# Kernel tuning notes

Measured on AMD Instinct MI355X. Metric: run time of the kernel, lower is better.

## Reference

```python
import jax, jax.numpy as jnp
import numpy as np

B_, NX, NY = 32, 512, 512


def _grad(f, axis):
    # torch.gradient(dim=axis, edge_order=2), unit spacing
    f = jnp.moveaxis(f, axis, -1)
    g = (jnp.roll(f, -1, axis=-1) - jnp.roll(f, 1, axis=-1)) * 0.5
    g0 = -1.5 * f[..., 0] + 2.0 * f[..., 1] - 0.5 * f[..., 2]
    gN = 1.5 * f[..., -1] - 2.0 * f[..., -2] + 0.5 * f[..., -3]
    g = g.at[..., 0].set(g0).at[..., -1].set(gN)
    return jnp.moveaxis(g, -1, axis)


def _grad2(f, axis):
    # roll-based 2nd derivative with one-sided 2nd-order boundary stencils
    f = jnp.moveaxis(f, axis, -1)
    g = jnp.roll(f, -1, axis=-1) - 2.0 * f + jnp.roll(f, 1, axis=-1)
    g0 = 2.0 * f[..., 0] - 5.0 * f[..., 1] + 4.0 * f[..., 2] - f[..., 3]
    gN = 2.0 * f[..., -1] - 5.0 * f[..., -2] + 4.0 * f[..., -3] - f[..., -4]
    g = g.at[..., 0].set(g0).at[..., -1].set(gN)
    return jnp.moveaxis(g, -1, axis)


def setup_inputs() -> dict:
    key = jax.random.key(0)
    k1, k2, k3, k4 = jax.random.split(key, 4)
    f = jax.random.uniform(k1, (B_, NX, NY), dtype=jnp.float32)
    dt = jax.random.uniform(k2, (B_,), dtype=jnp.float32)
    A = jax.random.normal(k3, (B_, 2, NX, NY), dtype=jnp.float32)
    B = jax.random.normal(k4, (B_, 3, NX, NY), dtype=jnp.float32)
    return {"f": f, "dt": dt, "A": A, "B": B}


def reference(f, dt, A, B):
    # Fokker-Planck explicit update: f' = f + dt * (-div(Af) + 0.5 * div^2(Bf))
    Af = A * f[:, None]            # [B, 2, Nx, Ny]
    Bf = B * f[:, None]            # [B, 3, Nx, Ny]
    gradv_Af = _grad(Af[:, 0], 1) + _grad(Af[:, 1], 2)
    gradvv_Bf = (_grad2(Bf[:, 0], 1) + _grad2(Bf[:, 1], 2)
                 + _grad(_grad(Bf[:, 2], 2), 1)
                 + _grad(_grad(Bf[:, 2], 1), 2))
    df = -gradv_Af + gradvv_Bf * 0.5
    f_new = f + df * dt[:, None, None]
    return jnp.maximum(f_new, 0.0)  # ensure_non_negative_f
```

## Files before the change

### kernel.cpp

```cpp
#include <hip/hip_runtime.h>


constexpr int NXc = 512;
constexpr int NYc = 512;
constexpr int NBc = 32;

struct Win { float m1, v0, v1, v2, v3, p4; };

__device__ __forceinline__ float4 mul4(float4 p, float4 q) {
    float4 r; r.x = p.x*q.x; r.y = p.y*q.y; r.z = p.z*q.z; r.w = p.w*q.w; return r;
}
__device__ __forceinline__ float4 fma4s(float s, float4 p, float4 acc) {
    acc.x = fmaf(s, p.x, acc.x); acc.y = fmaf(s, p.y, acc.y);
    acc.z = fmaf(s, p.z, acc.z); acc.w = fmaf(s, p.w, acc.w); return acc;
}
__device__ __forceinline__ float4 add4(float4 a, float4 b) {
    float4 r; r.x = a.x+b.x; r.y = a.y+b.y; r.z = a.z+b.z; r.w = a.w+b.w; return r;
}

__device__ __forceinline__ Win mkwin(float4 a, float am1, float ap4,
                                     float4 fv, float fm1, float fp4) {
    Win w;
    w.m1 = am1 * fm1;
    w.v0 = a.x * fv.x; w.v1 = a.y * fv.y; w.v2 = a.z * fv.z; w.v3 = a.w * fv.w;
    w.p4 = ap4 * fp4;
    return w;
}

__device__ __forceinline__ float4 dy4(const Win& w, bool atY0, bool atYN) {
    float4 r;
    r.x = atY0 ? (-1.5f*w.v0 + 2.0f*w.v1 - 0.5f*w.v2) : 0.5f*(w.v1 - w.m1);
    r.y = 0.5f*(w.v2 - w.v0);
    r.z = 0.5f*(w.v3 - w.v1);
    r.w = atYN ? (1.5f*w.v3 - 2.0f*w.v2 + 0.5f*w.v1) : 0.5f*(w.p4 - w.v2);
    return r;
}
__device__ __forceinline__ float4 dyy4(const Win& w, bool atY0, bool atYN) {
    float4 r;
    r.x = atY0 ? (2.0f*w.v0 - 5.0f*w.v1 + 4.0f*w.v2 - w.v3) : (w.v1 - 2.0f*w.v0 + w.m1);
    r.y = w.v2 - 2.0f*w.v1 + w.v0;
    r.z = w.v3 - 2.0f*w.v2 + w.v1;
    r.w = atYN ? (2.0f*w.v3 - 5.0f*w.v2 + 4.0f*w.v1 - w.v0) : (w.p4 - 2.0f*w.v3 + w.v2);
    return r;
}

__global__ __launch_bounds__(128) void fp2d_kernel(
    const float* __restrict__ f,
    const float* __restrict__ dt,
    const float* __restrict__ A,
    const float* __restrict__ Bm,
    float* __restrict__ out)
{
    const int x  = blockIdx.x & (NXc - 1);
    const int b  = blockIdx.x >> 9;
    const int y4 = threadIdx.x << 2;

    const bool atY0 = (y4 == 0);
    const bool atYN = (y4 == NYc - 4);
    const int ym1 = atY0 ? 0 : y4 - 1;
    const int yp4 = atYN ? NYc - 1 : y4 + 4;

    const size_t plane = (size_t)NXc * NYc;
    const float* fb = f  + (size_t)b * plane;
    const float* A0 = A  + (size_t)b * 2 * plane;
    const float* A1 = A0 + plane;
    const float* B0 = Bm + (size_t)b * 3 * plane;
    const float* B1 = B0 + plane;
    const float* B2 = B1 + plane;

    int xa, xb_, xc, u3; float wxa, wxb, wxc, v0, v1, v2, v3;
    if (x == 0) {
        xa = 0; xb_ = 1; xc = 2; u3 = 3;
        wxa = -1.5f; wxb = 2.0f; wxc = -0.5f;
        v0 = 2.0f; v1 = -5.0f; v2 = 4.0f; v3 = -1.0f;
    } else if (x == NXc - 1) {
        xa = NXc - 1; xb_ = NXc - 2; xc = NXc - 3; u3 = NXc - 4;
        wxa = 1.5f; wxb = -2.0f; wxc = 0.5f;
        v0 = 2.0f; v1 = -5.0f; v2 = 4.0f; v3 = -1.0f;
    } else {
        xa = x - 1; xb_ = x; xc = x + 1; u3 = x;
        wxa = -0.5f; wxb = 0.0f; wxc = 0.5f;
        v0 = 1.0f; v1 = -2.0f; v2 = 1.0f; v3 = 0.0f;
    }
    const bool xInt = (x > 0) && (x < NXc - 1);

    auto ld4 = [](const float* p, int row, int col) -> float4 {
        return *reinterpret_cast<const float4*>(p + (size_t)row * NYc + col);
    };
    auto ld1 = [](const float* p, int row, int col) -> float {
        return p[(size_t)row * NYc + col];
    };

    float4 f_a = ld4(fb, xa, y4);  float fam = ld1(fb, xa, ym1), fap = ld1(fb, xa, yp4);
    float4 f_b = ld4(fb, xb_, y4); float fbm = ld1(fb, xb_, ym1), fbp = ld1(fb, xb_, yp4);
    float4 f_c = ld4(fb, xc, y4);  float fcm = ld1(fb, xc, ym1), fcp = ld1(fb, xc, yp4);
    float4 f_u = ld4(fb, u3, y4);

    float4 fX = xInt ? f_b : f_a;
    float  fXm = xInt ? fbm : fam;
    float  fXp = xInt ? fbp : fap;

    float4 a0a = ld4(A0, xa, y4), a0b = ld4(A0, xb_, y4), a0c = ld4(A0, xc, y4);
    float4 a1x = ld4(A1, x,  y4); float a1m = ld1(A1, x, ym1), a1p = ld1(A1, x, yp4);

    float4 b0a = ld4(B0, xa, y4), b0b = ld4(B0, xb_, y4), b0c = ld4(B0, xc, y4), b0u = ld4(B0, u3, y4);
    float4 b1x = ld4(B1, x,  y4); float b1m = ld1(B1, x, ym1), b1p = ld1(B1, x, yp4);

    float4 b2a = ld4(B2, xa, y4);  float b2am = ld1(B2, xa, ym1), b2ap = ld1(B2, xa, yp4);
    float4 b2b = ld4(B2, xb_, y4); float b2bm = ld1(B2, xb_, ym1), b2bp = ld1(B2, xb_, yp4);
    float4 b2c = ld4(B2, xc, y4);  float b2cm = ld1(B2, xc, ym1), b2cp = ld1(B2, xc, yp4);

    float4 zero; zero.x = zero.y = zero.z = zero.w = 0.0f;
    float4 gradv = fma4s(wxa, mul4(a0a, f_a),
                   fma4s(wxb, mul4(a0b, f_b),
                   fma4s(wxc, mul4(a0c, f_c), zero)));
    Win wA1 = mkwin(a1x, a1m, a1p, fX, fXm, fXp);
    gradv = add4(gradv, dy4(wA1, atY0, atYN));

    float4 dxx = fma4s(v0, mul4(b0a, f_a),
                 fma4s(v1, mul4(b0b, f_b),
                 fma4s(v2, mul4(b0c, f_c),
                 fma4s(v3, mul4(b0u, f_u), zero))));

    Win wB1 = mkwin(b1x, b1m, b1p, fX, fXm, fXp);
    float4 dyy = dyy4(wB1, atY0, atYN);

    Win wB2a = mkwin(b2a, b2am, b2ap, f_a, fam, fap);
    Win wB2b = mkwin(b2b, b2bm, b2bp, f_b, fbm, fbp);
    Win wB2c = mkwin(b2c, b2cm, b2cp, f_c, fcm, fcp);
    float4 cross = fma4s(wxa, dy4(wB2a, atY0, atYN),
                   fma4s(wxb, dy4(wB2b, atY0, atYN),
                   fma4s(wxc, dy4(wB2c, atY0, atYN), zero)));

    const float dtb = dt[b];
    float4 res;
    {
        float dfx = 0.5f*(dxx.x + dyy.x) + cross.x - gradv.x;
        float dfy = 0.5f*(dxx.y + dyy.y) + cross.y - gradv.y;
        float dfz = 0.5f*(dxx.z + dyy.z) + cross.z - gradv.z;
        float dfw = 0.5f*(dxx.w + dyy.w) + cross.w - gradv.w;
        res.x = fmaxf(fmaf(dfx, dtb, fX.x), 0.0f);
        res.y = fmaxf(fmaf(dfy, dtb, fX.y), 0.0f);
        res.z = fmaxf(fmaf(dfz, dtb, fX.z), 0.0f);
        res.w = fmaxf(fmaf(dfw, dtb, fX.w), 0.0f);
    }

    *reinterpret_cast<float4*>(out + (size_t)b * plane + (size_t)x * NYc + y4) = res;
}

extern "C" void kernel_launch(void* const* d_in, const int* in_sizes, int n_in,
                              void* d_out, int out_size, void* d_ws, size_t ws_size,
                              hipStream_t stream) {
    const float* f  = (const float*)d_in[0];
    const float* dt = (const float*)d_in[1];
    const float* A  = (const float*)d_in[2];
    const float* Bm = (const float*)d_in[3];
    float* out = (float*)d_out;

    const int blocks = NBc * NXc;
    fp2d_kernel<<<blocks, 128, 0, stream>>>(f, dt, A, Bm, out);
}
```

Measured before the change: 238.5 us.

## Map one wavefront per row with 8 columns per lane and shuffle halos

Each 64-lane wavefront now covers a full 512-wide row, with each lane holding 8 contiguous columns, and a block of 256 threads covers 4 rows. Halo neighbours in y are exchanged with wavefront shuffles instead of extra scalar global loads, which removes about a dozen redundant scalar loads per thread. The block count drops by four and each thread keeps more data in registers, which raises register pressure. Edge lanes hold garbage shuffle values, but those are overridden by the one-sided boundary stencils.

```diff
diff --git a/kernel.cpp b/kernel.cpp
--- a/kernel.cpp
+++ b/kernel.cpp
@@ -5,7 +5,7 @@
 constexpr int NYc = 512;
 constexpr int NBc = 32;
 
-struct Win { float m1, v0, v1, v2, v3, p4; };
+struct F8 { float4 lo, hi; };
 
 __device__ __forceinline__ float4 mul4(float4 p, float4 q) {
     float4 r; r.x = p.x*q.x; r.y = p.y*q.y; r.z = p.z*q.z; r.w = p.w*q.w; return r;
@@ -14,51 +14,81 @@
     acc.x = fmaf(s, p.x, acc.x); acc.y = fmaf(s, p.y, acc.y);
     acc.z = fmaf(s, p.z, acc.z); acc.w = fmaf(s, p.w, acc.w); return acc;
 }
-__device__ __forceinline__ float4 add4(float4 a, float4 b) {
-    float4 r; r.x = a.x+b.x; r.y = a.y+b.y; r.z = a.z+b.z; r.w = a.w+b.w; return r;
+__device__ __forceinline__ F8 mul8(const F8& a, const F8& b) {
+    F8 r; r.lo = mul4(a.lo, b.lo); r.hi = mul4(a.hi, b.hi); return r;
+}
+__device__ __forceinline__ F8 fma8s(float s, const F8& p, const F8& acc) {
+    F8 r; r.lo = fma4s(s, p.lo, acc.lo); r.hi = fma4s(s, p.hi, acc.hi); return r;
+}
+__device__ __forceinline__ F8 add8(const F8& a, const F8& b) {
+    F8 r;
+    r.lo.x = a.lo.x+b.lo.x; r.lo.y = a.lo.y+b.lo.y; r.lo.z = a.lo.z+b.lo.z; r.lo.w = a.lo.w+b.lo.w;
+    r.hi.x = a.hi.x+b.hi.x; r.hi.y = a.hi.y+b.hi.y; r.hi.z = a.hi.z+b.hi.z; r.hi.w = a.hi.w+b.hi.w;
+    return r;
 }
 
-__device__ __forceinline__ Win mkwin(float4 a, float am1, float ap4,
-                                     float4 fv, float fm1, float fp4) {
-    Win w;
-    w.m1 = am1 * fm1;
-    w.v0 = a.x * fv.x; w.v1 = a.y * fv.y; w.v2 = a.z * fv.z; w.v3 = a.w * fv.w;
-    w.p4 = ap4 * fp4;
+__device__ __forceinline__ F8 ld8(const float* __restrict__ p, int row, int y8) {
+    const float* q = p + (size_t)row * NYc + y8;
+    F8 r;
+    r.lo = *reinterpret_cast<const float4*>(q);
+    r.hi = *reinterpret_cast<const float4*>(q + 4);
+    return r;
+}
+
+struct W8 { float4 lo, hi; float m1, p8; };
+
+__device__ __forceinline__ W8 mkwin8(const F8& a, const F8& f) {
+    W8 w;
+    w.lo = mul4(a.lo, f.lo);
+    w.hi = mul4(a.hi, f.hi);
+    w.m1 = __shfl_up(w.hi.w, 1);
+    w.p8 = __shfl_down(w.lo.x, 1);
     return w;
 }
 
-__device__ __forceinline__ float4 dy4(const Win& w, bool atY0, bool atYN) {
-    float4 r;
-    r.x = atY0 ? (-1.5f*w.v0 + 2.0f*w.v1 - 0.5f*w.v2) : 0.5f*(w.v1 - w.m1);
-    r.y = 0.5f*(w.v2 - w.v0);
-    r.z = 0.5f*(w.v3 - w.v1);
-    r.w = atYN ? (1.5f*w.v3 - 2.0f*w.v2 + 0.5f*w.v1) : 0.5f*(w.p4 - w.v2);
+__device__ __forceinline__ F8 dy8(const W8& w, bool atY0, bool atYN) {
+    F8 r;
+    r.lo.x = atY0 ? (-1.5f*w.lo.x + 2.0f*w.lo.y - 0.5f*w.lo.z) : 0.5f*(w.lo.y - w.m1);
+    r.lo.y = 0.5f*(w.lo.z - w.lo.x);
+    r.lo.z = 0.5f*(w.lo.w - w.lo.y);
+    r.lo.w = 0.5f*(w.hi.x - w.lo.z);
+    r.hi.x = 0.5f*(w.hi.y - w.lo.w);
+    r.hi.y = 0.5f*(w.hi.z - w.hi.x);
+    r.hi.z = 0.5f*(w.hi.w - w.hi.y);
+    r.hi.w = atYN ? (1.5f*w.hi.w - 2.0f*w.hi.z + 0.5f*w.hi.y) : 0.5f*(w.p8 - w.hi.z);
     return r;
 }
-__device__ __forceinline__ float4 dyy4(const Win& w, bool atY0, bool atYN) {
-    float4 r;
-    r.x = atY0 ? (2.0f*w.v0 - 5.0f*w.v1 + 4.0f*w.v2 - w.v3) : (w.v1 - 2.0f*w.v0 + w.m1);
-    r.y = w.v2 - 2.0f*w.v1 + w.v0;
-    r.z = w.v3 - 2.0f*w.v2 + w.v1;
-    r.w = atYN ? (2.0f*w.v3 - 5.0f*w.v2 + 4.0f*w.v1 - w.v0) : (w.p4 - 2.0f*w.v3 + w.v2);
+__device__ __forceinline__ F8 dyy8(const W8& w, bool atY0, bool atYN) {
+    F8 r;
+    r.lo.x = atY0 ? (2.0f*w.lo.x - 5.0f*w.lo.y + 4.0f*w.lo.z - w.lo.w)
+                  : (w.lo.y - 2.0f*w.lo.x + w.m1);
+    r.lo.y = w.lo.z - 2.0f*w.lo.y + w.lo.x;
+    r.lo.z = w.lo.w - 2.0f*w.lo.z + w.lo.y;
+    r.lo.w = w.hi.x - 2.0f*w.lo.w + w.lo.z;
+    r.hi.x = w.hi.y - 2.0f*w.hi.x + w.lo.w;
+    r.hi.y = w.hi.z - 2.0f*w.hi.y + w.hi.x;
+    r.hi.z = w.hi.w - 2.0f*w.hi.z + w.hi.y;
+    r.hi.w = atYN ? (2.0f*w.hi.w - 5.0f*w.hi.z + 4.0f*w.hi.y - w.hi.x)
+                  : (w.p8 - 2.0f*w.hi.w + w.hi.z);
     return r;
 }
 
-__global__ __launch_bounds__(128) void fp2d_kernel(
+__global__ __launch_bounds__(256) void fp2d_kernel(
     const float* __restrict__ f,
     const float* __restrict__ dt,
     const float* __restrict__ A,
     const float* __restrict__ Bm,
     float* __restrict__ out)
 {
-    const int x  = blockIdx.x & (NXc - 1);
-    const int b  = blockIdx.x >> 9;
-    const int y4 = threadIdx.x << 2;
+    const int tid  = threadIdx.x;
+    const int wv   = tid >> 6;
+    const int lane = tid & 63;
+    const int b    = blockIdx.x >> 7;
+    const int x    = ((blockIdx.x & 127) << 2) + wv;
+    const int y8   = lane << 3;
 
-    const bool atY0 = (y4 == 0);
-    const bool atYN = (y4 == NYc - 4);
-    const int ym1 = atY0 ? 0 : y4 - 1;
-    const int yp4 = atYN ? NYc - 1 : y4 + 4;
+    const bool atY0 = (lane == 0);
+    const bool atYN = (lane == 63);
 
     const size_t plane = (size_t)NXc * NYc;
     const float* fb = f  + (size_t)b * plane;
@@ -84,68 +114,59 @@
     }
     const bool xInt = (x > 0) && (x < NXc - 1);
 
-    auto ld4 = [](const float* p, int row, int col) -> float4 {
-        return *reinterpret_cast<const float4*>(p + (size_t)row * NYc + col);
-    };
-    auto ld1 = [](const float* p, int row, int col) -> float {
-        return p[(size_t)row * NYc + col];
-    };
+    F8 f_a = ld8(fb, xa, y8);
+    F8 f_b = ld8(fb, xb_, y8);
+    F8 f_c = ld8(fb, xc, y8);
+    F8 f_u = ld8(fb, u3, y8);
 
-    float4 f_a = ld4(fb, xa, y4);  float fam = ld1(fb, xa, ym1), fap = ld1(fb, xa, yp4);
-    float4 f_b = ld4(fb, xb_, y4); float fbm = ld1(fb, xb_, ym1), fbp = ld1(fb, xb_, yp4);
-    float4 f_c = ld4(fb, xc, y4);  float fcm = ld1(fb, xc, ym1), fcp = ld1(fb, xc, yp4);
-    float4 f_u = ld4(fb, u3, y4);
+    F8 a0a = ld8(A0, xa, y8), a0b = ld8(A0, xb_, y8), a0c = ld8(A0, xc, y8);
+    F8 a1x = ld8(A1, x, y8);
+    F8 b0a = ld8(B0, xa, y8), b0b = ld8(B0, xb_, y8), b0c = ld8(B0, xc, y8), b0u = ld8(B0, u3, y8);
+    F8 b1x = ld8(B1, x, y8);
+    F8 b2a = ld8(B2, xa, y8), b2b = ld8(B2, xb_, y8), b2c = ld8(B2, xc, y8);
 
-    float4 fX = xInt ? f_b : f_a;
-    float  fXm = xInt ? fbm : fam;
-    float  fXp = xInt ? fbp : fap;
+    F8 fX;
+    fX.lo = xInt ? f_b.lo : f_a.lo;
+    fX.hi = xInt ? f_b.hi : f_a.hi;
 
-    float4 a0a = ld4(A0, xa, y4), a0b = ld4(A0, xb_, y4), a0c = ld4(A0, xc, y4);
-    float4 a1x = ld4(A1, x,  y4); float a1m = ld1(A1, x, ym1), a1p = ld1(A1, x, yp4);
+    F8 zero8; zero8.lo = make_float4(0.f,0.f,0.f,0.f); zero8.hi = zero8.lo;
 
-    float4 b0a = ld4(B0, xa, y4), b0b = ld4(B0, xb_, y4), b0c = ld4(B0, xc, y4), b0u = ld4(B0, u3, y4);
-    float4 b1x = ld4(B1, x,  y4); float b1m = ld1(B1, x, ym1), b1p = ld1(B1, x, yp4);
+    F8 gradv = fma8s(wxa, mul8(a0a, f_a),
+               fma8s(wxb, mul8(a0b, f_b),
+               fma8s(wxc, mul8(a0c, f_c), zero8)));
+    W8 wA1 = mkwin8(a1x, fX);
+    gradv = add8(gradv, dy8(wA1, atY0, atYN));
 
-    float4 b2a = ld4(B2, xa, y4);  float b2am = ld1(B2, xa, ym1), b2ap = ld1(B2, xa, yp4);
-    float4 b2b = ld4(B2, xb_, y4); float b2bm = ld1(B2, xb_, ym1), b2bp = ld1(B2, xb_, yp4);
-    float4 b2c = ld4(B2, xc, y4);  float b2cm = ld1(B2, xc, ym1), b2cp = ld1(B2, xc, yp4);
+    F8 dxx = fma8s(v0, mul8(b0a, f_a),
+             fma8s(v1, mul8(b0b, f_b),
+             fma8s(v2, mul8(b0c, f_c),
+             fma8s(v3, mul8(b0u, f_u), zero8))));
 
-    float4 zero; zero.x = zero.y = zero.z = zero.w = 0.0f;
-    float4 gradv = fma4s(wxa, mul4(a0a, f_a),
-                   fma4s(wxb, mul4(a0b, f_b),
-                   fma4s(wxc, mul4(a0c, f_c), zero)));
-    Win wA1 = mkwin(a1x, a1m, a1p, fX, fXm, fXp);
-    gradv = add4(gradv, dy4(wA1, atY0, atYN));
+    W8 wB1 = mkwin8(b1x, fX);
+    F8 dyy = dyy8(wB1, atY0, atYN);
 
-    float4 dxx = fma4s(v0, mul4(b0a, f_a),
-                 fma4s(v1, mul4(b0b, f_b),
-                 fma4s(v2, mul4(b0c, f_c),
-                 fma4s(v3, mul4(b0u, f_u), zero))));
-
-    Win wB1 = mkwin(b1x, b1m, b1p, fX, fXm, fXp);
-    float4 dyy = dyy4(wB1, atY0, atYN);
-
-    Win wB2a = mkwin(b2a, b2am, b2ap, f_a, fam, fap);
-    Win wB2b = mkwin(b2b, b2bm, b2bp, f_b, fbm, fbp);
-    Win wB2c = mkwin(b2c, b2cm, b2cp, f_c, fcm, fcp);
-    float4 cross = fma4s(wxa, dy4(wB2a, atY0, atYN),
-                   fma4s(wxb, dy4(wB2b, atY0, atYN),
-                   fma4s(wxc, dy4(wB2c, atY0, atYN), zero)));
+    W8 wB2a = mkwin8(b2a, f_a);
+    W8 wB2b = mkwin8(b2b, f_b);
+    W8 wB2c = mkwin8(b2c, f_c);
+    F8 cross = fma8s(wxa, dy8(wB2a, atY0, atYN),
+               fma8s(wxb, dy8(wB2b, atY0, atYN),
+               fma8s(wxc, dy8(wB2c, atY0, atYN), zero8)));
 
     const float dtb = dt[b];
-    float4 res;
-    {
-        float dfx = 0.5f*(dxx.x + dyy.x) + cross.x - gradv.x;
-        float dfy = 0.5f*(dxx.y + dyy.y) + cross.y - gradv.y;
-        float dfz = 0.5f*(dxx.z + dyy.z) + cross.z - gradv.z;
-        float dfw = 0.5f*(dxx.w + dyy.w) + cross.w - gradv.w;
-        res.x = fmaxf(fmaf(dfx, dtb, fX.x), 0.0f);
-        res.y = fmaxf(fmaf(dfy, dtb, fX.y), 0.0f);
-        res.z = fmaxf(fmaf(dfz, dtb, fX.z), 0.0f);
-        res.w = fmaxf(fmaf(dfw, dtb, fX.w), 0.0f);
-    }
+    float* orow = out + (size_t)b * plane + (size_t)x * NYc + y8;
 
-    *reinterpret_cast<float4*>(out + (size_t)b * plane + (size_t)x * NYc + y4) = res;
+    float4 r0, r1;
+    r0.x = fmaxf(fmaf(0.5f*(dxx.lo.x + dyy.lo.x) + cross.lo.x - gradv.lo.x, dtb, fX.lo.x), 0.0f);
+    r0.y = fmaxf(fmaf(0.5f*(dxx.lo.y + dyy.lo.y) + cross.lo.y - gradv.lo.y, dtb, fX.lo.y), 0.0f);
+    r0.z = fmaxf(fmaf(0.5f*(dxx.lo.z + dyy.lo.z) + cross.lo.z - gradv.lo.z, dtb, fX.lo.z), 0.0f);
+    r0.w = fmaxf(fmaf(0.5f*(dxx.lo.w + dyy.lo.w) + cross.lo.w - gradv.lo.w, dtb, fX.lo.w), 0.0f);
+    r1.x = fmaxf(fmaf(0.5f*(dxx.hi.x + dyy.hi.x) + cross.hi.x - gradv.hi.x, dtb, fX.hi.x), 0.0f);
+    r1.y = fmaxf(fmaf(0.5f*(dxx.hi.y + dyy.hi.y) + cross.hi.y - gradv.hi.y, dtb, fX.hi.y), 0.0f);
+    r1.z = fmaxf(fmaf(0.5f*(dxx.hi.z + dyy.hi.z) + cross.hi.z - gradv.hi.z, dtb, fX.hi.z), 0.0f);
+    r1.w = fmaxf(fmaf(0.5f*(dxx.hi.w + dyy.hi.w) + cross.hi.w - gradv.hi.w, dtb, fX.hi.w), 0.0f);
+
+    *reinterpret_cast<float4*>(orow)     = r0;
+    *reinterpret_cast<float4*>(orow + 4) = r1;
 }
 
 extern "C" void kernel_launch(void* const* d_in, const int* in_sizes, int n_in,
@@ -157,6 +178,6 @@
     const float* Bm = (const float*)d_in[3];
     float* out = (float*)d_out;
 
-    const int blocks = NBc * NXc;
-    fp2d_kernel<<<blocks, 128, 0, stream>>>(f, dt, A, Bm, out);
+    const int blocks = NBc * NXc / 4;
+    fp2d_kernel<<<blocks, 256, 0, stream>>>(f, dt, A, Bm, out);
 }
```

Result: faster. 218.5 us (-8.4%).
